# Kernel tuning notes

Measured on AMD Instinct MI355X. Metric: run time of the kernel, lower is better.

Reference implementation:

```python
import jax, jax.numpy as jnp
import numpy as np
from jax import lax

TEMP = 0.1  # softmax_temp default in forward


def _conv(x, w, b):
    y = lax.conv_general_dilated(x, w, (1, 1), 'VALID',
                                 dimension_numbers=('NCHW', 'OIHW', 'NCHW'))
    return y + b[None, :, None, None]


def _avg_pool2(x):
    # AvgPool2d(2,2), floor mode (VALID window)
    s = lax.reduce_window(x, 0.0, lax.add, (1, 1, 2, 2), (1, 1, 2, 2), 'VALID')
    return s / 4.0


def _cnn(x, c1w, c1b, c2w, c2b, c3w, c3b, dw, db):
    x = _avg_pool2(jax.nn.relu(_conv(x, c1w, c1b)))   # (N,8,13,13)
    x = _avg_pool2(jax.nn.relu(_conv(x, c2w, c2b)))   # (N,16,5,5)
    x = _avg_pool2(jax.nn.relu(_conv(x, c3w, c3b)))   # (N,32,1,1)
    x = x.reshape(x.shape[0], -1)                      # (N,32)
    logits = x @ dw.T + db                             # (N,10)
    return jax.nn.softmax(logits, axis=1)


def _digit_to_rule(p):
    # p: (N,10) -> (N,6)
    return jnp.stack([p[:, 8], p[:, 4] + p[:, 6], p[:, 0] + p[:, 2],
                      p[:, 7] + p[:, 9], p[:, 5], p[:, 1] + p[:, 3]], axis=1)


def setup_inputs() -> dict:
    key = jax.random.key(0)
    ks = jax.random.split(key, 10)
    B, T, D, C, H, W = 256, 8, 4, 1, 28, 28
    sc = 0.1
    return {
        'sequences': jax.random.normal(ks[0], (B, T, D, C, H, W), jnp.float32),
        'conv1_w': jax.random.normal(ks[1], (8, 1, 3, 3), jnp.float32) * sc,
        'conv1_b': jax.random.normal(ks[2], (8,), jnp.float32) * sc,
        'conv2_w': jax.random.normal(ks[3], (16, 8, 3, 3), jnp.float32) * sc,
        'conv2_b': jax.random.normal(ks[4], (16,), jnp.float32) * sc,
        'conv3_w': jax.random.normal(ks[5], (32, 16, 3, 3), jnp.float32) * sc,
        'conv3_b': jax.random.normal(ks[6], (32,), jnp.float32) * sc,
        'dense_w': jax.random.normal(ks[7], (10, 32), jnp.float32) * sc,
        'dense_b': jax.random.normal(ks[8], (10,), jnp.float32) * sc,
        'trans': jax.nn.softmax(jax.random.normal(ks[9], (6, 9, 10), jnp.float32), axis=-1),
    }


def reference(sequences, conv1_w, conv1_b, conv2_w, conv2_b, conv3_w, conv3_b,
              dense_w, dense_b, trans):
    B, T, D, C, H, W = sequences.shape
    S = trans.shape[2]           # num_states = 10
    N = T * D                    # number of recurrence steps
    # CNN is independent per (t,d,b): batch all images at once.
    imgs = jnp.transpose(sequences, (1, 2, 0, 3, 4, 5)).reshape(N * B, C, H, W)
    digit_probs = _cnn(imgs, conv1_w, conv1_b, conv2_w, conv2_b,
                       conv3_w, conv3_b, dense_w, dense_b)      # (N*B,10)
    guard_probs = _digit_to_rule(digit_probs)                   # (N*B,6)

    # Per-rule transition matrices: softmax with temperature + fixed accepting row.
    M = jax.nn.softmax(trans / TEMP, axis=-1)                   # (R,S-1,S)
    acc = jnp.zeros((S,), M.dtype).at[-1].set(1.0)
    M = jnp.concatenate([M, jnp.broadcast_to(acc, (M.shape[0], 1, S))], axis=1)  # (R,S,S)

    # Effective transition matrices per step and batch element.
    g = guard_probs.reshape(N, B, -1)
    A_all = jnp.einsum('nbr,rij->nbij', g, M)                   # (N,B,S,S)

    state0 = jnp.zeros((B, S), sequences.dtype).at[:, 0].set(1.0)

    def step(state, A):
        return jnp.einsum('bi,bij->bj', state, A), None

    state_final, _ = lax.scan(step, state0, A_all)
    all_cnn_preds = digit_probs.reshape(N, B, -1)
    all_guard_preds = g
    return all_cnn_preds, all_guard_preds, state_final
```

## Files before the change

### kernel.cpp

```cpp
#include <hip/hip_runtime.h>

typedef _Float16 half_t;
typedef _Float16 h2 __attribute__((ext_vector_type(2)));
typedef _Float16 h4 __attribute__((ext_vector_type(4)));
typedef _Float16 f16x8 __attribute__((ext_vector_type(8)));
typedef float f32x4 __attribute__((ext_vector_type(4)));

__device__ __forceinline__ float fdot2f(h2 a, h2 b, float c) {
#if __has_builtin(__builtin_amdgcn_fdot2)
    return __builtin_amdgcn_fdot2(a, b, c, false);
#else
    return c + (float)a.x * (float)b.x + (float)a.y * (float)b.y;
#endif
}

__global__ __launch_bounds__(256) void prep_kernel(
    const float* __restrict__ w2g, const float* __restrict__ w3g,
    const float* __restrict__ wdg, float* __restrict__ wsW)
{
    const int tid = threadIdx.x;
    half_t* w3h = (half_t*)(wsW + 320);
    half_t* w2B = (half_t*)(wsW + 2624);
    for (int i = tid; i < 320; i += 256) {
        int j = i >> 5, c2 = i & 31;
        wsW[c2 * 10 + j] = wdg[i];
    }
    for (int i = tid; i < 4608; i += 256) {
        int l = i & 3, c = (i >> 2) & 31, g = (i >> 7) & 3, k = i >> 9;
        w3h[i] = (half_t)w3g[(c * 16 + g * 4 + l) * 9 + k];
    }
    for (int i = tid; i < 1536; i += 256) {
        int c    = i >> 9;
        int r    = i & 511;
        int lane = r >> 3;
        int j    = r & 7;
        int k    = c * 32 + ((lane >> 4) << 3) + j;
        half_t val = (half_t)0.f;
        if (k < 72) {
            int t = k >> 2, l = k & 3;
            int g = (t >= 9) ? 1 : 0;
            int tap = t - 9 * g;
            int oc  = lane & 15;
            val = (half_t)w2g[(oc * 8 + g * 4 + l) * 9 + tap];
        }
        w2B[i] = val;
    }
}

__global__ __launch_bounds__(256, 4) void cnn_kernel(
    const float* __restrict__ seq,
    const float* __restrict__ w1g, const float* __restrict__ b1g,
    const float* __restrict__ b2g, const float* __restrict__ b3g,
    const float* __restrict__ bdg, const float* __restrict__ wsW,
    float* __restrict__ out)
{
    __shared__ __align__(16) float  s_img2[4][28][28];
    __shared__ __align__(16) half_t s_p1n[4][2][10][11][4];
    __shared__ __align__(16) half_t s_p2n[4][16][16];
    __shared__ __align__(16) half_t s_w[4608];
    __shared__ float s_p3[4][32];

    const int tid   = threadIdx.x;
    const int mbase = blockIdx.x * 4;
    const float*  wdt = wsW;
    const half_t* w2B = (const half_t*)(wsW + 2624);

    {
        const float4* wsrc = (const float4*)(wsW + 320);
        float4* wdst = (float4*)s_w;
        for (int i = tid; i < 576; i += 256) wdst[i] = wsrc[i];
    }
    if (tid < 196) {
        #pragma unroll
        for (int img = 0; img < 4; img++) {
            const int m = mbase + img;
            const int b = m & 255, nn = m >> 8;
            const int t = nn >> 2, dd = nn & 3;
            const float4* s4 = (const float4*)(seq + (((size_t)b * 8 + t) * 4 + dd) * 784);
            float4 v = s4[tid];
            int flat = tid * 4;
            int r  = flat / 28;
            int cb = flat - r * 28;
            int e  = cb >> 1;
            *(float2*)&s_img2[img][r][e]      = make_float2(v.x, v.z);
            *(float2*)&s_img2[img][r][14 + e] = make_float2(v.y, v.w);
        }
    }
    __syncthreads();

    for (int idx = tid; idx < 400; idx += 256) {
        const int img = idx / 100;
        const int rem = idx - img * 100;
        const int y   = rem / 10;
        const int x   = rem - y * 10;
        const int r0  = 2 * y;
        float p[4][4];
        #pragma unroll
        for (int i = 0; i < 4; i++) {
            const float* rp = &s_img2[img][r0 + i][0];
            p[i][0] = rp[x];
            p[i][1] = rp[14 + x];
            p[i][2] = rp[x + 1];
            p[i][3] = rp[15 + x];
        }
        float res[8];
        #pragma unroll
        for (int c = 0; c < 8; c++) {
            float w[9];
            #pragma unroll
            for (int k = 0; k < 9; k++) w[k] = w1g[c * 9 + k];
            const float bias = b1g[c];
            float acc = 0.f;
            #pragma unroll
            for (int rr = 0; rr < 2; rr++)
                #pragma unroll
                for (int cc = 0; cc < 2; cc++) {
                    float v = bias;
                    #pragma unroll
                    for (int i = 0; i < 3; i++)
                        #pragma unroll
                        for (int j = 0; j < 3; j++)
                            v += p[rr + i][cc + j] * w[i * 3 + j];
                    acc += fmaxf(v, 0.f);
                }
            res[c] = 0.25f * acc;
        }
        const int slot = (x >> 1) + 5 * (x & 1);
        h4 lo = { (half_t)res[0], (half_t)res[1], (half_t)res[2], (half_t)res[3] };
        h4 hi = { (half_t)res[4], (half_t)res[5], (half_t)res[6], (half_t)res[7] };
        *(h4*)&s_p1n[img][0][y][slot][0] = lo;
        *(h4*)&s_p1n[img][1][y][slot][0] = hi;
    }
    __syncthreads();

    const int img2 = tid >> 6;
    const int t6   = tid & 63;

    {
        const int q  = t6 >> 4;
        const int oc = t6 & 15;
        int tg[6], ti[6], tj[6];
        bool tv[6];
        #pragma unroll
        for (int c = 0; c < 3; c++)
            #pragma unroll
            for (int s = 0; s < 2; s++) {
                int e = c * 2 + s;
                int t = c * 8 + q * 2 + s;
                bool v = (t < 18);
                int tt = v ? t : 0;
                int g = (tt >= 9) ? 1 : 0;
                int tap = tt - 9 * g;
                tg[e] = g; ti[e] = tap / 3; tj[e] = tap - 3 * (tap / 3); tv[e] = v;
            }
        f16x8 B[3];
        #pragma unroll
        for (int c = 0; c < 3; c++)
            B[c] = *(const f16x8*)&w2B[(c * 64 + t6) * 8];

        const float bias = b2g[oc];
        f32x4 acc[4];
        #pragma unroll
        for (int T = 0; T < 4; T++) {
            acc[T][0] = bias; acc[T][1] = bias; acc[T][2] = bias; acc[T][3] = bias;
        }
        const int mm = t6 & 15;
        #pragma unroll
        for (int T = 0; T < 4; T++) {
            const int cy = 2 * T + (mm >> 3);
            const int cx = mm & 7;
            #pragma unroll
            for (int c = 0; c < 3; c++) {
                h4 a0, a1;
                a0[0]=a0[1]=a0[2]=a0[3]=(half_t)0.f;
                a1[0]=a1[1]=a1[2]=a1[3]=(half_t)0.f;
                const int e0 = c * 2, e1 = c * 2 + 1;
                if (tv[e0]) {
                    int col = cx + tj[e0];
                    int slot = (col >> 1) + 5 * (col & 1);
                    a0 = *(const h4*)&s_p1n[img2][tg[e0]][cy + ti[e0]][slot][0];
                }
                if (tv[e1]) {
                    int col = cx + tj[e1];
                    int slot = (col >> 1) + 5 * (col & 1);
                    a1 = *(const h4*)&s_p1n[img2][tg[e1]][cy + ti[e1]][slot][0];
                }
                f16x8 A = __builtin_shufflevector(a0, a1, 0, 1, 2, 3, 4, 5, 6, 7);
                acc[T] = __builtin_amdgcn_mfma_f32_16x16x32_f16(A, B[c], acc[T], 0, 0, 0);
            }
        }
        #pragma unroll
        for (int T = 0; T < 4; T++) {
            float p0 = fmaxf(acc[T][0], 0.f) + fmaxf(acc[T][1], 0.f);
            float p1 = fmaxf(acc[T][2], 0.f) + fmaxf(acc[T][3], 0.f);
            p0 += __shfl_xor(p0, 32, 64);
            p1 += __shfl_xor(p1, 32, 64);
            if (q < 2) {
                s_p2n[img2][T * 4 + q * 2    ][oc] = (half_t)(0.25f * p0);
                s_p2n[img2][T * 4 + q * 2 + 1][oc] = (half_t)(0.25f * p1);
            }
        }
    }
    __syncthreads();

    {
        const int c = t6 >> 1;
        const int u = t6 & 1;
        float acc0 = b3g[c], acc1 = acc0;
        #pragma unroll
        for (int g = 0; g < 4; g++) {
            h2 AL[3][4], AH[3][4];
            #pragma unroll
            for (int i = 0; i < 3; i++)
                #pragma unroll
                for (int jj = 0; jj < 4; jj++) {
                    h4 a = *(const h4*)&s_p2n[img2][(u + i) * 4 + jj][g * 4];
                    AL[i][jj] = __builtin_shufflevector(a, a, 0, 1);
                    AH[i][jj] = __builtin_shufflevector(a, a, 2, 3);
                }
            h4 wk[9];
            #pragma unroll
            for (int k = 0; k < 9; k++)
                wk[k] = *(const h4*)&s_w[((k * 4 + g) * 32 + c) * 4];
            #pragma unroll
            for (int k = 0; k < 9; k++) {
                const int i = k / 3, j = k - i * 3;
                h2 wL = __builtin_shufflevector(wk[k], wk[k], 0, 1);
                h2 wH = __builtin_shufflevector(wk[k], wk[k], 2, 3);
                acc0 = fdot2f(AL[i][j], wL, acc0);
                acc0 = fdot2f(AH[i][j], wH, acc0);
                acc1 = fdot2f(AL[i][j + 1], wL, acc1);
                acc1 = fdot2f(AH[i][j + 1], wH, acc1);
            }
        }
        float s = fmaxf(acc0, 0.f) + fmaxf(acc1, 0.f);
        s += __shfl_xor(s, 1, 64);
        if (u == 0) s_p3[img2][c] = 0.25f * s;
    }
    __syncthreads();

    {
        float logit = -1e30f;
        if (t6 < 10) {
            float acc = bdg[t6];
            #pragma unroll
            for (int c2 = 0; c2 < 32; c2++) acc += s_p3[img2][c2] * wdt[c2 * 10 + t6];
            logit = acc;
        }
        float mx = logit;
        #pragma unroll
        for (int s = 1; s < 16; s <<= 1) mx = fmaxf(mx, __shfl_xor(mx, s, 16));
        float e = (t6 < 10) ? __expf(logit - mx) : 0.f;
        float ssum = e;
        #pragma unroll
        for (int s = 1; s < 16; s <<= 1) ssum += __shfl_xor(ssum, s, 16);
        float p = e / ssum;
        const int m = mbase + img2;
        if (t6 < 10) out[(size_t)m * 10 + t6] = p;

        const int sh = (t6 < 6 ? t6 : 0) * 4;
        const int ia = (0x157048 >> sh) & 0xF;
        const int ib = (0x3F926F >> sh) & 0xF;
        float pa = __shfl(p, ia, 16);
        float pb = __shfl(p, ib, 16);
        if (t6 < 6)
            out[81920 + (size_t)m * 6 + t6] = pa + pb;
    }
}

__global__ __launch_bounds__(256) void sfa_kernel(
    const float* __restrict__ trans,
    const float* __restrict__ out_guards,
    float* __restrict__ out)
{
    __shared__ float M[600];
    const int tid  = threadIdx.x;
    const int lane = tid & 63;
    const int wv   = tid >> 6;

    if (tid < 54) {
        int r = tid / 9, i = tid - r * 9;
        const float* row = trans + (size_t)(r * 9 + i) * 10;
        float x[10], mx = -1e30f;
        #pragma unroll
        for (int j = 0; j < 10; j++) { x[j] = 10.f * row[j]; mx = fmaxf(mx, x[j]); }
        float s = 0.f;
        #pragma unroll
        for (int j = 0; j < 10; j++) { x[j] = __expf(x[j] - mx); s += x[j]; }
        float inv = 1.f / s;
        #pragma unroll
        for (int j = 0; j < 10; j++) M[(r * 9 + i) * 10 + j] = x[j] * inv;
    }
    __syncthreads();

    const int bb    = lane / 10;
    const int j     = lane - bb * 10;
    const int base  = bb * 10;
    const bool ok   = (bb < 6);
    int batch = blockIdx.x * 24 + wv * 6 + bb;
    const bool live = ok && (batch < 256);
    if (!live) batch = 0;

    float Mreg[54];
    #pragma unroll
    for (int k = 0; k < 54; k++) Mreg[k] = M[k * 10 + j];

    float stj = (j == 0) ? 1.f : 0.f;
    const float* gbase = out_guards + 81920;

    for (int nn = 0; nn < 32; nn++) {
        const float* gp = gbase + ((size_t)nn * 256 + batch) * 6;
        float2 ga = *(const float2*)(gp);
        float2 gb = *(const float2*)(gp + 2);
        float2 gc = *(const float2*)(gp + 4);
        float g[6] = {ga.x, ga.y, gb.x, gb.y, gc.x, gc.y};

        float st[10];
        #pragma unroll
        for (int i = 0; i < 10; i++) st[i] = __shfl(stj, base + i, 64);

        float gsum = g[0] + g[1] + g[2] + g[3] + g[4] + g[5];
        float ns = (j == 9) ? gsum * st[9] : 0.f;
        #pragma unroll
        for (int r = 0; r < 6; r++) {
            float h = 0.f;
            #pragma unroll
            for (int i = 0; i < 9; i++) h += st[i] * Mreg[r * 9 + i];
            ns += g[r] * h;
        }
        stj = ns;
    }
    if (live) out[131072 + (size_t)batch * 10 + j] = stj;
}

extern "C" void kernel_launch(void* const* d_in, const int* in_sizes, int n_in,
                              void* d_out, int out_size, void* d_ws, size_t ws_size,
                              hipStream_t stream) {
    const float* seq = (const float*)d_in[0];
    const float* w1  = (const float*)d_in[1];
    const float* b1  = (const float*)d_in[2];
    const float* w2  = (const float*)d_in[3];
    const float* b2  = (const float*)d_in[4];
    const float* w3  = (const float*)d_in[5];
    const float* b3  = (const float*)d_in[6];
    const float* wd  = (const float*)d_in[7];
    const float* bd  = (const float*)d_in[8];
    const float* tr  = (const float*)d_in[9];
    float* out = (float*)d_out;
    float* wsW = (float*)d_ws;

    prep_kernel<<<1, 256, 0, stream>>>(w2, w3, wd, wsW);
    cnn_kernel<<<2048, 256, 0, stream>>>(seq, w1, b1, b2, b3, bd, wsW, out);
    sfa_kernel<<<11, 256, 0, stream>>>(tr, out, out);
}
```

Baseline: 136.1 us.

## Compute conv3 with MFMA using pre-swizzled global weights, drop shared weight staging

Replaces the per-thread fdot2 implementation of the third convolution with 16x16x32 f16 MFMA instructions run by two wavefronts. Each wavefront covers 16 output channels across the four images and their four pooling windows, and reads weights pre-laid out by the prep kernel directly from global memory. The shared-memory copy of conv3 weights goes away, and the occupancy hint rises from 4 to 6 blocks per CU. In exchange, only two of the four wavefronts do work in this stage, and the weight operands are now fetched from global memory instead of LDS.

```diff
diff --git a/kernel.cpp b/kernel.cpp
--- a/kernel.cpp
+++ b/kernel.cpp
@@ -6,28 +6,16 @@
 typedef _Float16 f16x8 __attribute__((ext_vector_type(8)));
 typedef float f32x4 __attribute__((ext_vector_type(4)));
 
-__device__ __forceinline__ float fdot2f(h2 a, h2 b, float c) {
-#if __has_builtin(__builtin_amdgcn_fdot2)
-    return __builtin_amdgcn_fdot2(a, b, c, false);
-#else
-    return c + (float)a.x * (float)b.x + (float)a.y * (float)b.y;
-#endif
-}
-
 __global__ __launch_bounds__(256) void prep_kernel(
     const float* __restrict__ w2g, const float* __restrict__ w3g,
     const float* __restrict__ wdg, float* __restrict__ wsW)
 {
     const int tid = threadIdx.x;
-    half_t* w3h = (half_t*)(wsW + 320);
-    half_t* w2B = (half_t*)(wsW + 2624);
+    half_t* w2B = (half_t*)(wsW + 320);
+    half_t* w3B = (half_t*)(wsW + 1088);
     for (int i = tid; i < 320; i += 256) {
         int j = i >> 5, c2 = i & 31;
         wsW[c2 * 10 + j] = wdg[i];
-    }
-    for (int i = tid; i < 4608; i += 256) {
-        int l = i & 3, c = (i >> 2) & 31, g = (i >> 7) & 3, k = i >> 9;
-        w3h[i] = (half_t)w3g[(c * 16 + g * 4 + l) * 9 + k];
     }
     for (int i = tid; i < 1536; i += 256) {
         int c    = i >> 9;
@@ -45,9 +33,24 @@
         }
         w2B[i] = val;
     }
+    for (int i = tid; i < 5120; i += 256) {
+        int j    = i & 7;
+        int lane = (i >> 3) & 63;
+        int tc   = i >> 9;
+        int tile = tc / 5;
+        int c    = tc - tile * 5;
+        int k    = c * 32 + ((lane >> 4) << 3) + j;
+        int n    = lane & 15;
+        half_t val = (half_t)0.f;
+        if (k < 144) {
+            int ic = k & 15, tap = k >> 4;
+            val = (half_t)w3g[((tile * 16 + n) * 16 + ic) * 9 + tap];
+        }
+        w3B[i] = val;
+    }
 }
 
-__global__ __launch_bounds__(256, 4) void cnn_kernel(
+__global__ __launch_bounds__(256, 6) void cnn_kernel(
     const float* __restrict__ seq,
     const float* __restrict__ w1g, const float* __restrict__ b1g,
     const float* __restrict__ b2g, const float* __restrict__ b3g,
@@ -57,19 +60,14 @@
     __shared__ __align__(16) float  s_img2[4][28][28];
     __shared__ __align__(16) half_t s_p1n[4][2][10][11][4];
     __shared__ __align__(16) half_t s_p2n[4][16][16];
-    __shared__ __align__(16) half_t s_w[4608];
     __shared__ float s_p3[4][32];
 
     const int tid   = threadIdx.x;
     const int mbase = blockIdx.x * 4;
     const float*  wdt = wsW;
-    const half_t* w2B = (const half_t*)(wsW + 2624);
-
-    {
-        const float4* wsrc = (const float4*)(wsW + 320);
-        float4* wdst = (float4*)s_w;
-        for (int i = tid; i < 576; i += 256) wdst[i] = wsrc[i];
-    }
+    const half_t* w2B = (const half_t*)(wsW + 320);
+    const half_t* w3B = (const half_t*)(wsW + 1088);
+
     if (tid < 196) {
         #pragma unroll
         for (int img = 0; img < 4; img++) {
@@ -172,8 +170,8 @@
             #pragma unroll
             for (int c = 0; c < 3; c++) {
                 h4 a0, a1;
-                a0[0]=a0[1]=a0[2]=a0[3]=(half_t)0.f;
-                a1[0]=a1[1]=a1[2]=a1[3]=(half_t)0.f;
+                #pragma unroll
+                for (int z = 0; z < 4; z++) { a0[z] = (half_t)0.f; a1[z] = (half_t)0.f; }
                 const int e0 = c * 2, e1 = c * 2 + 1;
                 if (tv[e0]) {
                     int col = cx + tj[e0];
@@ -203,39 +201,38 @@
     }
     __syncthreads();
 
-    {
-        const int c = t6 >> 1;
-        const int u = t6 & 1;
-        float acc0 = b3g[c], acc1 = acc0;
-        #pragma unroll
-        for (int g = 0; g < 4; g++) {
-            h2 AL[3][4], AH[3][4];
-            #pragma unroll
-            for (int i = 0; i < 3; i++)
+    if ((tid >> 6) < 2) {
+        const int tile = tid >> 6;
+        const int lane = tid & 63;
+        const int n    = lane & 15;
+        const int quad = lane >> 4;
+        const int oc   = tile * 16 + n;
+        const int am   = lane & 15;
+        const int aimg = am >> 2;
+        const int awin = am & 3;
+        const int au   = awin >> 1, av = awin & 1;
+        const int icb  = (quad & 1) * 8;
+
+        float bias = b3g[oc];
+        f32x4 acc;
+        acc[0] = bias; acc[1] = bias; acc[2] = bias; acc[3] = bias;
+        #pragma unroll
+        for (int c = 0; c < 5; c++) {
+            const int tap = c * 2 + (quad >> 1);
+            f16x8 A;
+            if (tap < 9) {
+                const int i = tap / 3, j = tap - 3 * i;
+                A = *(const f16x8*)&s_p2n[aimg][(au + i) * 4 + (av + j)][icb];
+            } else {
                 #pragma unroll
-                for (int jj = 0; jj < 4; jj++) {
-                    h4 a = *(const h4*)&s_p2n[img2][(u + i) * 4 + jj][g * 4];
-                    AL[i][jj] = __builtin_shufflevector(a, a, 0, 1);
-                    AH[i][jj] = __builtin_shufflevector(a, a, 2, 3);
-                }
-            h4 wk[9];
-            #pragma unroll
-            for (int k = 0; k < 9; k++)
-                wk[k] = *(const h4*)&s_w[((k * 4 + g) * 32 + c) * 4];
-            #pragma unroll
-            for (int k = 0; k < 9; k++) {
-                const int i = k / 3, j = k - i * 3;
-                h2 wL = __builtin_shufflevector(wk[k], wk[k], 0, 1);
-                h2 wH = __builtin_shufflevector(wk[k], wk[k], 2, 3);
-                acc0 = fdot2f(AL[i][j], wL, acc0);
-                acc0 = fdot2f(AH[i][j], wH, acc0);
-                acc1 = fdot2f(AL[i][j + 1], wL, acc1);
-                acc1 = fdot2f(AH[i][j + 1], wH, acc1);
+                for (int z = 0; z < 8; z++) A[z] = (half_t)0.f;
             }
-        }
-        float s = fmaxf(acc0, 0.f) + fmaxf(acc1, 0.f);
-        s += __shfl_xor(s, 1, 64);
-        if (u == 0) s_p3[img2][c] = 0.25f * s;
+            f16x8 B = *(const f16x8*)&w3B[((tile * 5 + c) * 64 + lane) * 8];
+            acc = __builtin_amdgcn_mfma_f32_16x16x32_f16(A, B, acc, 0, 0, 0);
+        }
+        float s = fmaxf(acc[0], 0.f) + fmaxf(acc[1], 0.f) +
+                  fmaxf(acc[2], 0.f) + fmaxf(acc[3], 0.f);
+        s_p3[quad][oc] = 0.25f * s;
     }
     __syncthreads();
 
```

After: 132.0 us. -3.0%, faster.
